# Performance work log

Measured on AMD Instinct MI355X. Metric: run time of the kernel, lower is better.

## Reference

```python
import jax, jax.numpy as jnp
import numpy as np

B, NA, NMAX, NC = 32, 8400, 32, 80
TOPK, ALPHA, BETA, EPS, BG_IDX = 13, 1.0, 6.0, 1e-9, 80
IMG = 640.0


def _ciou(box1, box2, eps=1e-7):
    # box1: (b, nmax, 1, 4) xyxy, box2: (b, 1, na, 4) xyxy -> CIoU (b, nmax, na)
    b1_x1, b1_y1, b1_x2, b1_y2 = (box1[..., 0], box1[..., 1], box1[..., 2], box1[..., 3])
    b2_x1, b2_y1, b2_x2, b2_y2 = (box2[..., 0], box2[..., 1], box2[..., 2], box2[..., 3])
    inter = (jnp.minimum(b1_x2, b2_x2) - jnp.maximum(b1_x1, b2_x1)).clip(0) * \
            (jnp.minimum(b1_y2, b2_y2) - jnp.maximum(b1_y1, b2_y1)).clip(0)
    w1, h1 = b1_x2 - b1_x1, b1_y2 - b1_y1 + eps
    w2, h2 = b2_x2 - b2_x1, b2_y2 - b2_y1 + eps
    union = w1 * h1 + w2 * h2 - inter + eps
    iou = inter / union
    cw = jnp.maximum(b1_x2, b2_x2) - jnp.minimum(b1_x1, b2_x1)
    ch = jnp.maximum(b1_y2, b2_y2) - jnp.minimum(b1_y1, b2_y1)
    c2 = cw * cw + ch * ch + eps
    rho2 = ((b2_x1 + b2_x2 - b1_x1 - b1_x2) ** 2 + (b2_y1 + b2_y2 - b1_y1 - b1_y2) ** 2) / 4.0
    v = (4.0 / np.pi ** 2) * (jnp.arctan(w2 / h2) - jnp.arctan(w1 / h1)) ** 2
    alpha = jax.lax.stop_gradient(v / (v - iou + (1.0 + eps)))
    return iou - (rho2 / c2 + v * alpha)


def _rand_boxes(key, shape):
    # well-formed xyxy boxes inside a 640x640 image
    k1, k2 = jax.random.split(key)
    xy = jax.random.uniform(k1, shape[:-1] + (2,), jnp.float32) * (IMG - 64.0)
    wh = jax.random.uniform(k2, shape[:-1] + (2,), jnp.float32) * 56.0 + 8.0
    return jnp.concatenate([xy, xy + wh], axis=-1)


def setup_inputs() -> dict:
    key = jax.random.key(0)
    ks = jax.random.split(key, 6)
    pd_scores = jax.random.uniform(ks[0], (B, NA, NC), jnp.float32)
    pd_bboxes = _rand_boxes(ks[1], (B, NA, 4))
    anc_points = jax.random.uniform(ks[2], (NA, 2), jnp.float32) * IMG
    gt_labels = jax.random.randint(ks[3], (B, NMAX, 1), 0, NC, dtype=jnp.int32)
    gt_bboxes = _rand_boxes(ks[4], (B, NMAX, 4))
    mask_gt = jnp.ones((B, NMAX, 1), jnp.float32)
    return {"pd_scores": pd_scores, "pd_bboxes": pd_bboxes, "anc_points": anc_points,
            "gt_labels": gt_labels, "gt_bboxes": gt_bboxes, "mask_gt": mask_gt}


def reference(pd_scores, pd_bboxes, anc_points, gt_labels, gt_bboxes, mask_gt):
    b, na, nc = pd_scores.shape
    nmax = gt_bboxes.shape[1]
    # pairwise CIoU between every GT and every predicted box: (b, nmax, na)
    overlaps = _ciou(gt_bboxes[:, :, None, :], pd_bboxes[:, None, :, :])
    # gather predicted class score at each GT's label: (b, nmax, na)
    p = jnp.transpose(pd_scores, (0, 2, 1))                     # (b, nc, na)
    scores = jnp.take_along_axis(p, gt_labels.astype(jnp.int32), axis=1)
    align_metric = (scores ** ALPHA) * (overlaps ** BETA)
    # top-k anchors per GT along the anchor axis, scatter to a boolean mask
    _, topk_idx = jax.lax.top_k(align_metric, TOPK)             # (b, nmax, topk)
    bi = jnp.arange(b)[:, None, None]
    gi = jnp.arange(nmax)[None, :, None]
    mask_pos = jnp.zeros((b, nmax, na), bool).at[bi, gi, topk_idx].set(True)
    target_gt_idx = jnp.argmax(mask_pos, axis=1)                # (b, na)
    fg_mask = mask_pos.sum(axis=1) > 0                          # (b, na)
    # gather assigned GT label / box per anchor
    target_labels = jnp.take_along_axis(gt_labels[..., 0].astype(jnp.int32), target_gt_idx, axis=1)
    target_bboxes = jnp.take_along_axis(gt_bboxes, target_gt_idx[..., None], axis=1)  # (b, na, 4)
    target_scores = jax.nn.one_hot(target_labels, nc, dtype=jnp.float32) * fg_mask[..., None]
    target_labels = jnp.where(fg_mask, target_labels, BG_IDX)
    # normalize target scores by mean positive overlap per anchor, clamped to [0, 1]
    mpf = mask_pos.astype(overlaps.dtype)
    pos_overlaps = jnp.clip((overlaps * mpf).sum(axis=1) / (mpf.sum(axis=1) + EPS), 0.0, 1.0)
    target_scores = target_scores * pos_overlaps[..., None]
    return target_labels, target_bboxes, target_scores, fg_mask, target_gt_idx
```

## Files before the change

kernel.cpp:

```cpp
#include <hip/hip_runtime.h>
#include <math.h>

#define BATCH 32
#define NA 8400
#define NMAX 32
#define NC 80
#define TOPK 13
#define THREADS 256
#define NF4ROW (NA / 4)
#define NPT4 9
#define TILE 128
#define NTILES 66
#define SSTRIDE 81

#define OFF_BOX 268800
#define OFF_SCR 1344000
#define OFF_FG  22848000
#define OFF_TGT 23116800
#define SCR_ELEMS (OFF_FG - OFF_SCR)
#define SCR_F4    (SCR_ELEMS / 4)
#define ZPB_M     2546

typedef float f32x4 __attribute__((ext_vector_type(4)));

__device__ __forceinline__ float ciou_f(float gx1, float gy1, float gx2, float gy2,
                                        float px1, float py1, float px2, float py2) {
    const float eps = 1e-7f;
    float iw = fmaxf(fminf(gx2, px2) - fmaxf(gx1, px1), 0.0f);
    float ih = fmaxf(fminf(gy2, py2) - fmaxf(gy1, py1), 0.0f);
    float inter = iw * ih;
    float w1 = gx2 - gx1, h1 = gy2 - gy1 + eps;
    float w2 = px2 - px1, h2 = py2 - py1 + eps;
    float uni = w1 * h1 + w2 * h2 - inter + eps;
    float iou = inter / uni;
    float cw = fmaxf(gx2, px2) - fminf(gx1, px1);
    float ch = fmaxf(gy2, py2) - fminf(gy1, py1);
    float c2 = cw * cw + ch * ch + eps;
    float dx = px1 + px2 - gx1 - gx2;
    float dy = py1 + py2 - gy1 - gy2;
    float rho2 = (dx * dx + dy * dy) / 4.0f;
    float dd = atanf(w2 / h2) - atanf(w1 / h1);
    float v = (float)(4.0 / (M_PI * M_PI)) * dd * dd;
    float alpha = v / (v - iou + (1.0f + eps));
    return iou - (rho2 / c2 + v * alpha);
}

__global__ __launch_bounds__(THREADS, 3) void metric_kernel(
    const float* __restrict__ pd_scores, const float* __restrict__ pd_bboxes,
    const int* __restrict__ gt_labels, const float* __restrict__ gt_bboxes,
    float* __restrict__ met, unsigned int* __restrict__ mask,
    float* __restrict__ zbase) {
    const int b = blockIdx.y;
    const int abase = blockIdx.x * TILE;
    const int tid = threadIdx.x;
    const int na_tile = min(TILE, NA - abase);
    const float eps = 1e-7f;

    if (tid < na_tile) mask[(size_t)b * NA + abase + tid] = 0u;

    __shared__ float ssc[TILE][SSTRIDE];
    __shared__ float4 spbox[TILE];
    __shared__ float sgx1[NMAX], sgy1[NMAX], sgx2[NMAX], sgy2[NMAX];
    __shared__ float sa1[NMAX], sat1[NMAX];
    __shared__ int   slbl[NMAX];

    if (tid < NMAX) {
        float4 g = ((const float4*)gt_bboxes)[b * NMAX + tid];
        float w1 = g.z - g.x, h1 = g.w - g.y + eps;
        sgx1[tid] = g.x; sgy1[tid] = g.y; sgx2[tid] = g.z; sgy2[tid] = g.w;
        sa1[tid]  = w1 * h1;
        sat1[tid] = atanf(w1 / h1);
        slbl[tid] = gt_labels[b * NMAX + tid];
    } else if (tid >= 128) {
        int al = tid - 128;
        if (al < na_tile)
            spbox[al] = ((const float4*)pd_bboxes)[(size_t)b * NA + abase + al];
    }

    const float4* srec4 = (const float4*)(pd_scores + ((size_t)b * NA + abase) * NC);
    const int nf4 = na_tile * 20;
    float4 r[10];
#pragma unroll
    for (int i = 0; i < 10; i++) {
        int f = tid + i * THREADS;
        if (f < nf4) r[i] = srec4[f];
    }
#pragma unroll
    for (int i = 0; i < 10; i++) {
        int f = tid + i * THREADS;
        if (f < nf4) {
            int a = f / 20, c = f % 20;
            float* d = &ssc[a][c * 4];
            d[0] = r[i].x; d[1] = r[i].y; d[2] = r[i].z; d[3] = r[i].w;
        }
    }
    __syncthreads();

    if (zbase) {
        const int bid = b * NTILES + blockIdx.x;
        const size_t zoff = (size_t)bid * ZPB_M;
        f32x4* zp = (f32x4*)zbase + zoff;
        const f32x4 z = { 0.f, 0.f, 0.f, 0.f };
#pragma unroll
        for (int i = 0; i < 10; i++) {
            int j = tid + i * THREADS;
            if (j < ZPB_M && zoff + j < SCR_F4)
                zp[j] = z;
        }
    }

    const int al = tid & (TILE - 1);
    const int gbase = (tid >> 7) * 16;
    if (al >= na_tile) return;

    float4 p = spbox[al];
    float w2 = p.z - p.x, h2 = p.w - p.y + eps;
    float a2  = w2 * h2;
    float at2 = atanf(w2 / h2);
    const size_t abs_a = (size_t)abase + al;

#pragma unroll
    for (int k = 0; k < 16; k++) {
        int gi = gbase + k;
        float gx1 = sgx1[gi], gy1 = sgy1[gi], gx2 = sgx2[gi], gy2 = sgy2[gi];
        float iw = fmaxf(fminf(gx2, p.z) - fmaxf(gx1, p.x), 0.0f);
        float ih = fmaxf(fminf(gy2, p.w) - fmaxf(gy1, p.y), 0.0f);
        float inter = iw * ih;
        float uni = sa1[gi] + a2 - inter + eps;
        float iou = inter / uni;
        float cw = fmaxf(gx2, p.z) - fminf(gx1, p.x);
        float ch = fmaxf(gy2, p.w) - fminf(gy1, p.y);
        float c2 = cw * cw + ch * ch + eps;
        float dx = p.x + p.z - gx1 - gx2;
        float dy = p.y + p.w - gy1 - gy2;
        float rho2 = (dx * dx + dy * dy) / 4.0f;
        float dd = at2 - sat1[gi];
        float v = (float)(4.0 / (M_PI * M_PI)) * dd * dd;
        float alpha = v / (v - iou + (1.0f + eps));
        float ov = iou - (rho2 / c2 + v * alpha);
        float sc = ssc[al][slbl[gi]];
        float ov2 = ov * ov;
        met[((size_t)b * NMAX + gi) * NA + abs_a] = sc * (ov2 * ov2 * ov2);
    }
}

__global__ __launch_bounds__(THREADS) void topk_kernel(
    const float* __restrict__ met, unsigned int* __restrict__ mask) {
    const int tid  = threadIdx.x;
    const int lane = tid & 63;
    const int w    = tid >> 6;
    const int bid  = blockIdx.x;
    const int b  = bid >> 5;
    const int gi = bid & 31;
    const f32x4* mrow4 = (const f32x4*)(met + ((size_t)b * NMAX + gi) * NA);

    f32x4 m4[NPT4];
#pragma unroll
    for (int j = 0; j < NPT4; j++) {
        int f = j * THREADS + tid;
        if (f < NF4ROW) m4[j] = mrow4[f];
    }

    float bv0 = -INFINITY, bv1 = -INFINITY;
    int   ba0 = 0x7FFFFFFF, ba1 = 0x7FFFFFFF;
#pragma unroll
    for (int j = 0; j < NPT4; j++) {
        int f = j * THREADS + tid;
        bool vf = (f < NF4ROW);
#pragma unroll
        for (int c = 0; c < 4; c++) {
            float v = vf ? m4[j][c] : -INFINITY;
            int   a = vf ? 4 * f + c : 0x7FFFFFFF;
            bool beats0 = (v > bv0) || (v == bv0 && a < ba0);
            bool beats1 = (v > bv1) || (v == bv1 && a < ba1);
            if (beats0) { bv1 = bv0; ba1 = ba0; bv0 = v; ba0 = a; }
            else if (beats1) { bv1 = v; ba1 = a; }
        }
    }
    bool valid1 = true;

    float rv = -INFINITY; int ra = 0x7FFFFFFF;
    for (int k = 0; k < TOPK; k++) {
        float v = bv0; int a = ba0;
#pragma unroll
        for (int s = 1; s < 64; s <<= 1) {
            float ov = __shfl_xor(v, s);
            int   oa = __shfl_xor(a, s);
            if (ov > v || (ov == v && oa < a)) { v = ov; a = oa; }
        }
        if (lane == k) { rv = v; ra = a; }
        if (ba0 == a) {
            if (valid1) { bv0 = bv1; ba0 = ba1; valid1 = false; }
            else {
                float nv = -INFINITY; int na_ = 0x7FFFFFFF;
#pragma unroll
                for (int j = 0; j < NPT4; j++) {
                    int f = j * THREADS + tid;
                    bool vf = (f < NF4ROW);
#pragma unroll
                    for (int c = 0; c < 4; c++) {
                        float mv = vf ? m4[j][c] : -INFINITY;
                        int   ma = vf ? 4 * f + c : 0x7FFFFFFF;
                        bool below = (mv < v) || (mv == v && ma > a);
                        bool beats = (mv > nv) || (mv == nv && ma < na_);
                        if (below && beats && vf) { nv = mv; na_ = ma; }
                    }
                }
                bv0 = nv; ba0 = na_;
            }
        }
    }

    __shared__ float lv[4 * TOPK];
    __shared__ int   la[4 * TOPK];
    if (lane < TOPK) { lv[w * TOPK + lane] = rv; la[w * TOPK + lane] = ra; }
    __syncthreads();

    if (w == 0) {
        float v = (lane < 4 * TOPK) ? lv[lane] : -INFINITY;
        int   a = (lane < 4 * TOPK) ? la[lane] : 0x7FFFFFFF;
        for (int k = 0; k < TOPK; k++) {
            float wv = v; int wa = a;
#pragma unroll
            for (int s = 1; s < 64; s <<= 1) {
                float ov = __shfl_xor(wv, s);
                int   oa = __shfl_xor(wa, s);
                if (ov > wv || (ov == wv && oa < wa)) { wv = ov; wa = oa; }
            }
            if (lane == 0) atomicOr(&mask[(size_t)b * NA + wa], 1u << gi);
            if (a == wa) { v = -INFINITY; a = 0x7FFFFFFF; }
        }
    }
}

__global__ __launch_bounds__(THREADS) void zero_scr_kernel(float* __restrict__ out) {
    f32x4* p = (f32x4*)(out + OFF_SCR);
    const f32x4 z = { 0.f, 0.f, 0.f, 0.f };
    const int stride = gridDim.x * THREADS;
    for (int i = blockIdx.x * THREADS + threadIdx.x; i < SCR_F4; i += stride)
        __builtin_nontemporal_store(z, p + i);
}

__global__ __launch_bounds__(THREADS) void assign_kernel(
    const float* __restrict__ pd_bboxes, const int* __restrict__ gt_labels,
    const float* __restrict__ gt_bboxes, const unsigned int* __restrict__ mask,
    float* __restrict__ out) {
    const int idx = blockIdx.x * THREADS + threadIdx.x;
    const int b = idx / NA;

    unsigned msk = mask[idx];
    int tgt = msk ? (__ffs(msk) - 1) : 0;
    float4 gb = ((const float4*)gt_bboxes)[b * NMAX + tgt];
    int lbl = gt_labels[b * NMAX + tgt];
    float4 p = ((const float4*)pd_bboxes)[idx];

    float sum = 0.0f;
    int cnt = 0;
    unsigned mm = msk;
    while (mm) {
        int i = __ffs(mm) - 1;
        mm &= mm - 1;
        float4 g = ((const float4*)gt_bboxes)[b * NMAX + i];
        sum += ciou_f(g.x, g.y, g.z, g.w, p.x, p.y, p.z, p.w);
        cnt++;
    }
    float po = fminf(fmaxf(sum / ((float)cnt + 1e-9f), 0.0f), 1.0f);

    bool fg = (msk != 0);
    __builtin_nontemporal_store(fg ? (float)lbl : 80.0f, &out[idx]);
    f32x4 gbv = { gb.x, gb.y, gb.z, gb.w };
    __builtin_nontemporal_store(gbv, (f32x4*)(out + OFF_BOX) + idx);
    __builtin_nontemporal_store(fg ? 1.0f : 0.0f, &out[OFF_FG + idx]);
    __builtin_nontemporal_store((float)tgt, &out[OFF_TGT + idx]);
    if (fg) out[OFF_SCR + (size_t)idx * NC + lbl] = po;
}

extern "C" void kernel_launch(void* const* d_in, const int* in_sizes, int n_in,
                              void* d_out, int out_size, void* d_ws, size_t ws_size,
                              hipStream_t stream) {
    const float* pd_scores = (const float*)d_in[0];
    const float* pd_bboxes = (const float*)d_in[1];
    const int*   gt_labels = (const int*)d_in[3];
    const float* gt_bboxes = (const float*)d_in[4];

    float* out = (float*)d_out;
    unsigned int* mask = (unsigned int*)d_ws;

    const size_t MASK_BYTES = (size_t)BATCH * NA * 4;
    const size_t MET_BYTES  = (size_t)BATCH * NMAX * NA * 4;
    const size_t met_off = (MASK_BYTES + 255) & ~(size_t)255;
    const bool ws_met = (ws_size >= met_off + MET_BYTES);

    float* met = ws_met ? (float*)((char*)d_ws + met_off) : out + OFF_SCR;

    dim3 g1(NTILES, BATCH);
    if (ws_met) {
        metric_kernel<<<g1, THREADS, 0, stream>>>(pd_scores, pd_bboxes,
                                                  gt_labels, gt_bboxes, met, mask,
                                                  out + OFF_SCR);
        topk_kernel<<<BATCH * NMAX, THREADS, 0, stream>>>(met, mask);
    } else {
        metric_kernel<<<g1, THREADS, 0, stream>>>(pd_scores, pd_bboxes,
                                                  gt_labels, gt_bboxes, met, mask,
                                                  nullptr);
        topk_kernel<<<BATCH * NMAX, THREADS, 0, stream>>>(met, mask);
        zero_scr_kernel<<<2048, THREADS, 0, stream>>>(out);
    }
    assign_kernel<<<BATCH * NA / THREADS, THREADS, 0, stream>>>(
        pd_bboxes, gt_labels, gt_bboxes, mask, out);
}
```

Before: 80.67 us.

## Retile metric kernel to 4 anchors x 4 GTs per thread with float4 stores

Each thread of the metric kernel now computes a 4-anchor by 4-GT block rather than 16 GTs for a single anchor, and writes each GT row as a float4 store. The per-anchor area and atan values are computed once per tile into shared memory, so each thread no longer recomputes them. The goal is fewer store instructions and less shared-memory reloading of GT parameters. In exchange it adds an extra barrier, and the strided ssc reads across four anchors may cause bank conflicts.

```diff
diff --git a/kernel.cpp b/kernel.cpp
--- a/kernel.cpp
+++ b/kernel.cpp
@@ -60,6 +60,7 @@
 
     __shared__ float ssc[TILE][SSTRIDE];
     __shared__ float4 spbox[TILE];
+    __shared__ float sa2_[TILE], sat2_[TILE];
     __shared__ float sgx1[NMAX], sgy1[NMAX], sgx2[NMAX], sgy2[NMAX];
     __shared__ float sa1[NMAX], sat1[NMAX];
     __shared__ int   slbl[NMAX];
@@ -85,6 +86,15 @@
         int f = tid + i * THREADS;
         if (f < nf4) r[i] = srec4[f];
     }
+    __syncthreads();
+
+    if (tid < na_tile) {
+        float4 p = spbox[tid];
+        float w2 = p.z - p.x, h2 = p.w - p.y + eps;
+        sa2_[tid]  = w2 * h2;
+        sat2_[tid] = atanf(w2 / h2);
+    }
+
 #pragma unroll
     for (int i = 0; i < 10; i++) {
         int f = tid + i * THREADS;
@@ -94,7 +104,6 @@
             d[0] = r[i].x; d[1] = r[i].y; d[2] = r[i].z; d[3] = r[i].w;
         }
     }
-    __syncthreads();
 
     if (zbase) {
         const int bid = b * NTILES + blockIdx.x;
@@ -108,39 +117,51 @@
                 zp[j] = z;
         }
     }
-
-    const int al = tid & (TILE - 1);
-    const int gbase = (tid >> 7) * 16;
-    if (al >= na_tile) return;
-
-    float4 p = spbox[al];
-    float w2 = p.z - p.x, h2 = p.w - p.y + eps;
-    float a2  = w2 * h2;
-    float at2 = atanf(w2 / h2);
-    const size_t abs_a = (size_t)abase + al;
-
-#pragma unroll
-    for (int k = 0; k < 16; k++) {
-        int gi = gbase + k;
-        float gx1 = sgx1[gi], gy1 = sgy1[gi], gx2 = sgx2[gi], gy2 = sgy2[gi];
-        float iw = fmaxf(fminf(gx2, p.z) - fmaxf(gx1, p.x), 0.0f);
-        float ih = fmaxf(fminf(gy2, p.w) - fmaxf(gy1, p.y), 0.0f);
-        float inter = iw * ih;
-        float uni = sa1[gi] + a2 - inter + eps;
-        float iou = inter / uni;
-        float cw = fmaxf(gx2, p.z) - fminf(gx1, p.x);
-        float ch = fmaxf(gy2, p.w) - fminf(gy1, p.y);
-        float c2 = cw * cw + ch * ch + eps;
-        float dx = p.x + p.z - gx1 - gx2;
-        float dy = p.y + p.w - gy1 - gy2;
-        float rho2 = (dx * dx + dy * dy) / 4.0f;
-        float dd = at2 - sat1[gi];
-        float v = (float)(4.0 / (M_PI * M_PI)) * dd * dd;
-        float alpha = v / (v - iou + (1.0f + eps));
-        float ov = iou - (rho2 / c2 + v * alpha);
-        float sc = ssc[al][slbl[gi]];
-        float ov2 = ov * ov;
-        met[((size_t)b * NMAX + gi) * NA + abs_a] = sc * (ov2 * ov2 * ov2);
+    __syncthreads();
+
+    const int q  = tid & 31;
+    const int g0 = (tid >> 5) * 4;
+    const int a0 = q * 4;
+    if (a0 >= na_tile) return;
+
+    float4 P[4]; float A2[4], AT2[4];
+#pragma unroll
+    for (int j = 0; j < 4; j++) {
+        P[j]   = spbox[a0 + j];
+        A2[j]  = sa2_[a0 + j];
+        AT2[j] = sat2_[a0 + j];
+    }
+
+#pragma unroll
+    for (int g = 0; g < 4; g++) {
+        const int gi = g0 + g;
+        const float gx1 = sgx1[gi], gy1 = sgy1[gi], gx2 = sgx2[gi], gy2 = sgy2[gi];
+        const float ga1 = sa1[gi], gat1 = sat1[gi];
+        const int   lbl = slbl[gi];
+        float4 mv;
+#pragma unroll
+        for (int j = 0; j < 4; j++) {
+            float4 p = P[j];
+            float iw = fmaxf(fminf(gx2, p.z) - fmaxf(gx1, p.x), 0.0f);
+            float ih = fmaxf(fminf(gy2, p.w) - fmaxf(gy1, p.y), 0.0f);
+            float inter = iw * ih;
+            float uni = ga1 + A2[j] - inter + eps;
+            float iou = inter / uni;
+            float cw = fmaxf(gx2, p.z) - fminf(gx1, p.x);
+            float ch = fmaxf(gy2, p.w) - fminf(gy1, p.y);
+            float c2 = cw * cw + ch * ch + eps;
+            float dx = p.x + p.z - gx1 - gx2;
+            float dy = p.y + p.w - gy1 - gy2;
+            float rho2 = (dx * dx + dy * dy) / 4.0f;
+            float dd = AT2[j] - gat1;
+            float v = (float)(4.0 / (M_PI * M_PI)) * dd * dd;
+            float alpha = v / (v - iou + (1.0f + eps));
+            float ov = iou - (rho2 / c2 + v * alpha);
+            float sc = ssc[a0 + j][lbl];
+            float ov2 = ov * ov;
+            ((float*)&mv)[j] = sc * (ov2 * ov2 * ov2);
+        }
+        ((float4*)(met + ((size_t)b * NMAX + gi) * NA + abase))[q] = mv;
     }
 }
 
```

After: 79.27 us. Within noise of the previous version (-1.7%).
